# Optimization experiments

Hardware: AMD Instinct MI355X
Metric: run time of the kernel (lower is better)

## Reference

```python
import jax, jax.numpy as jnp
import numpy as np

D = 256      # model_dim
H = 8        # num_heads
S = 256      # tokens per channel
CH = [4, 2, 6, 4]  # multiplex_channels_per_sample


def _make_padding(ch, s):
    # Build gather indices / mask mapping packed tokens [T] -> padded [B, Lmax]
    B = len(ch)
    lens = [c * s for c in ch]
    T = sum(lens)
    Lmax = max(lens)
    pad_idx = np.zeros((B, Lmax), dtype=np.int32)
    pad_mask = np.zeros((B, Lmax), dtype=bool)
    off = 0
    for b, L in enumerate(lens):
        pad_idx[b, :L] = np.arange(off, off + L, dtype=np.int32)
        pad_mask[b, :L] = True
        off += L
    return jnp.asarray(pad_idx), jnp.asarray(pad_mask)


def setup_inputs() -> dict:
    key = jax.random.key(0)
    ks = jax.random.split(key, 16)
    C = sum(CH)
    x_query = jax.random.normal(ks[0], (C, S, D), jnp.float32)
    x_keyval = jax.random.normal(ks[1], (C, S, D), jnp.float32)
    pos = jax.random.normal(ks[2], (C, S, D), jnp.float32)
    pad_idx, pad_mask = _make_padding(CH, S)
    sc = 1.0 / np.sqrt(D)
    Wq = jax.random.normal(ks[3], (D, D), jnp.float32) * sc
    Wk = jax.random.normal(ks[4], (D, D), jnp.float32) * sc
    Wv = jax.random.normal(ks[5], (D, D), jnp.float32) * sc
    Wo = jax.random.normal(ks[6], (D, D), jnp.float32) * sc
    bq = jax.random.normal(ks[7], (D,), jnp.float32) * 0.02
    bk = jax.random.normal(ks[8], (D,), jnp.float32) * 0.02
    bv = jax.random.normal(ks[9], (D,), jnp.float32) * 0.02
    bo = jax.random.normal(ks[10], (D,), jnp.float32) * 0.02
    return {"x_query": x_query, "x_keyval": x_keyval, "pos": pos,
            "pad_idx": pad_idx, "pad_mask": pad_mask,
            "Wq": Wq, "bq": bq, "Wk": Wk, "bk": bk,
            "Wv": Wv, "bv": bv, "Wo": Wo, "bo": bo}


def reference(x_query, x_keyval, pos, pad_idx, pad_mask,
              Wq, bq, Wk, bk, Wv, bv, Wo, bo):
    C, s, d = x_query.shape
    T = C * s
    dh = d // H
    # MHA with positional embedding: pos is added to query and key inputs
    # (query_pos = key_pos = pos in the original forward), value is raw.
    q_in = (x_query + pos).reshape(T, d)
    k_in = (x_keyval + pos).reshape(T, d)
    v_in = x_keyval.reshape(T, d)
    q = q_in @ Wq + bq
    k = k_in @ Wk + bk
    v = v_in @ Wv + bv
    # Pad packed ragged tokens into [B, Lmax, D] per cu_seq_len segments
    B, Lmax = pad_idx.shape
    qp = q[pad_idx].reshape(B, Lmax, H, dh)
    kp = k[pad_idx].reshape(B, Lmax, H, dh)
    vp = v[pad_idx].reshape(B, Lmax, H, dh)
    scores = jnp.einsum('bqhd,bkhd->bhqk', qp, kp) / jnp.sqrt(jnp.asarray(dh, q.dtype))
    neg = jnp.asarray(jnp.finfo(scores.dtype).min, scores.dtype)
    scores = jnp.where(pad_mask[:, None, None, :], scores, neg)
    attn = jax.nn.softmax(scores, axis=-1)
    out = jnp.einsum('bhqk,bkhd->bqhd', attn, vp).reshape(B, Lmax, d)
    out = out * pad_mask[..., None]
    # Scatter padded outputs back to packed layout [T, D]
    flat = jnp.zeros((T, d), out.dtype).at[pad_idx.reshape(-1)].add(out.reshape(-1, d))
    flat = flat @ Wo + bo
    return flat.reshape(C, s, d)
```

## Files before the change

### kernel.cpp

```cpp
#include <hip/hip_runtime.h>
#include <math.h>

#define Dm 256
#define Tt 4096

typedef short  s16x8 __attribute__((ext_vector_type(8)));
typedef float  f32x4 __attribute__((ext_vector_type(4)));

__device__ __forceinline__ ushort f2bf(float x) {
    union { float f; unsigned u; } v; v.f = x;
    unsigned r = v.u + 0x7fffu + ((v.u >> 16) & 1u);
    return (ushort)(r >> 16);
}

__device__ __forceinline__ int ppos(int row, int key) {
    return row * 64 + (key & 7) + ((((key >> 3) ^ (row >> 1)) & 7) << 3);
}

__global__ __launch_bounds__(256)
void convert_x(const float* __restrict__ xq, const float* __restrict__ xkv,
               const float* __restrict__ pos,
               ushort* __restrict__ A0, ushort* __restrict__ A1, ushort* __restrict__ A2)
{
    const int t = threadIdx.x;
    const int m = blockIdx.y;
    const float* xin = (m == 0) ? xq : xkv;
    ushort* out = (m == 0) ? A0 : (m == 1) ? A1 : A2;
    const int token = blockIdx.x * 32 + (t >> 3);
    const int c0 = (t & 7) * 32;
    const float* p = &xin[token * Dm + c0];
    const float* pp = &pos[token * Dm + c0];
    #pragma unroll
    for (int i = 0; i < 4; ++i) {
        float4 fa = *(const float4*)&p[i * 8];
        float4 fb = *(const float4*)&p[i * 8 + 4];
        if (m < 2) {
            float4 pa = *(const float4*)&pp[i * 8], pb = *(const float4*)&pp[i * 8 + 4];
            fa.x += pa.x; fa.y += pa.y; fa.z += pa.z; fa.w += pa.w;
            fb.x += pb.x; fb.y += pb.y; fb.z += pb.z; fb.w += pb.w;
        }
        s16x8 v8;
        v8[0] = (short)f2bf(fa.x); v8[1] = (short)f2bf(fa.y);
        v8[2] = (short)f2bf(fa.z); v8[3] = (short)f2bf(fa.w);
        v8[4] = (short)f2bf(fb.x); v8[5] = (short)f2bf(fb.y);
        v8[6] = (short)f2bf(fb.z); v8[7] = (short)f2bf(fb.w);
        *(s16x8*)&out[token * Dm + c0 + i * 8] = v8;
    }
}

__global__ __launch_bounds__(256)
void prep_w(const float* __restrict__ Wq, const float* __restrict__ Wk,
            const float* __restrict__ Wv, const float* __restrict__ Wo,
            ushort* __restrict__ Wt)
{
    __shared__ float T[64][65];
    const int tid = threadIdx.x;
    const int m = blockIdx.y;
    const int i = blockIdx.x >> 2, j = blockIdx.x & 3;
    const float* W = (m == 0) ? Wq : (m == 1) ? Wk : (m == 2) ? Wv : Wo;

    #pragma unroll
    for (int s = 0; s < 4; ++s) {
        int idx = s * 256 + tid;
        int r = idx >> 4, c4 = (idx & 15) << 2;
        float4 f = *(const float4*)&W[(i * 64 + r) * Dm + j * 64 + c4];
        T[c4 + 0][r] = f.x; T[c4 + 1][r] = f.y;
        T[c4 + 2][r] = f.z; T[c4 + 3][r] = f.w;
    }
    __syncthreads();
    #pragma unroll
    for (int s = 0; s < 2; ++s) {
        int idx = s * 256 + tid;
        int cr = idx >> 3, k8 = (idx & 7) << 3;
        s16x8 v8;
        #pragma unroll
        for (int jj = 0; jj < 8; ++jj) v8[jj] = (short)f2bf(T[cr][k8 + jj]);
        *(s16x8*)&Wt[m * 65536 + (j * 64 + cr) * Dm + i * 64 + k8] = v8;
    }
}

__global__ __launch_bounds__(256)
void proj_gemm(const ushort* __restrict__ A0, const ushort* __restrict__ A1,
               const ushort* __restrict__ A2, const ushort* __restrict__ Wt,
               const float* __restrict__ bq, const float* __restrict__ bk,
               const float* __restrict__ bv,
               ushort* __restrict__ qo, ushort* __restrict__ ko, ushort* __restrict__ vT)
{
    __shared__ __align__(16) ushort A_s[64 * 64];
    __shared__ __align__(16) ushort B_s[64 * 64];
    const int tid = threadIdx.x;
    const int lane = tid & 63, g = lane >> 4, myrow = lane & 15, w = tid >> 6;
    const int t0 = blockIdx.x * 64;
    const int c0 = blockIdx.y * 64;
    const int m  = blockIdx.z;
    const ushort* Ab = (m == 0) ? A0 : (m == 1) ? A1 : A2;
    const ushort* WT = Wt + m * 65536;
    const float* bias = (m == 0) ? bq : (m == 1) ? bk : bv;

    f32x4 acc[4] = {};
    for (int ks = 0; ks < 4; ++ks) {
        const int k0 = ks * 64;
        #pragma unroll
        for (int s = 0; s < 2; ++s) {
            int idx = s * 256 + tid;
            int r = idx >> 3, c = idx & 7;
            *(s16x8*)&A_s[r * 64 + ((c ^ (r & 7)) << 3)] =
                *(const s16x8*)&Ab[(t0 + r) * Dm + k0 + c * 8];
            *(s16x8*)&B_s[r * 64 + ((c ^ (r & 7)) << 3)] =
                *(const s16x8*)&WT[(c0 + r) * Dm + k0 + c * 8];
        }
        __syncthreads();
        const int arow = w * 16 + myrow;
        #pragma unroll
        for (int kk = 0; kk < 2; ++kk) {
            s16x8 a = *(s16x8*)&A_s[arow * 64 + (((g + 4 * kk) ^ (arow & 7)) << 3)];
            #pragma unroll
            for (int ct = 0; ct < 4; ++ct) {
                int brow = ct * 16 + myrow;
                s16x8 b = *(s16x8*)&B_s[brow * 64 + (((g + 4 * kk) ^ (brow & 7)) << 3)];
                acc[ct] = __builtin_amdgcn_mfma_f32_16x16x32_bf16(a, b, acc[ct], 0, 0, 0);
            }
        }
        __syncthreads();
    }
    const float qsc = 0.17677669529663687f;
    #pragma unroll
    for (int ct = 0; ct < 4; ++ct) {
        int col = c0 + ct * 16 + myrow;
        float bval = bias[col];
        #pragma unroll
        for (int r = 0; r < 4; ++r) {
            int tok = t0 + w * 16 + 4 * g + r;
            float vv = acc[ct][r] + bval;
            if (m == 0)      qo[tok * Dm + col] = f2bf(vv * qsc);
            else if (m == 1) ko[tok * Dm + col] = f2bf(vv);
            else             vT[col * Tt + tok] = f2bf(vv);
        }
    }
}

__global__ __launch_bounds__(256)
void attn2(const ushort* __restrict__ q, const ushort* __restrict__ kb,
           const ushort* __restrict__ vT, ushort* __restrict__ o)
{
    __shared__ __align__(16) ushort K_s[4][64 * 32];
    __shared__ __align__(16) ushort V_s[4][32 * 64];
    __shared__ __align__(16) ushort P_s[4][16 * 64];
    const int tid = threadIdx.x;
    const int lane = tid & 63, g = lane >> 4, myrow = lane & 15, w = tid >> 6;
    const int h = blockIdx.x & 7, qt = blockIdx.x >> 3;

    int off, L;
    if (qt < 32)      { off = 0;    L = 1024; }
    else if (qt < 48) { off = 1024; L = 512;  }
    else if (qt < 96) { off = 1536; L = 1536; }
    else              { off = 3072; L = 1024; }
    const int qrow0 = qt * 32;
    const int Lw = L >> 2;
    const int kbeg = off + w * Lw;
    const int nt = Lw >> 6;

    s16x8 qf[2];
    qf[0] = *(const s16x8*)&q[(qrow0 + myrow) * Dm + h * 32 + g * 8];
    qf[1] = *(const s16x8*)&q[(qrow0 + 16 + myrow) * Dm + h * 32 + g * 8];

    f32x4 aO[2][2] = {};
    float mr[2][4], lr[2][4];
    #pragma unroll
    for (int s = 0; s < 2; ++s)
        #pragma unroll
        for (int r = 0; r < 4; ++r) { mr[s][r] = -INFINITY; lr[s][r] = 0.f; }

    s16x8 kr[4], vr[4];
    #define LOAD_TILE(kc) do {                                                          \
        int kcc = (kc);                                                                 \
        _Pragma("unroll")                                                               \
        for (int i = 0; i < 4; ++i) {                                                   \
            int idx = i * 64 + lane;                                                    \
            kr[i] = *(const s16x8*)&kb[(kcc + (idx >> 2)) * Dm + h * 32 + ((idx & 3) << 3)]; \
            vr[i] = *(const s16x8*)&vT[(h * 32 + (lane >> 3) + i * 8) * Tt + kcc + ((lane & 7) << 3)]; \
        }                                                                               \
    } while (0)

    LOAD_TILE(kbeg);
    for (int t = 0; t < nt; ++t) {
        asm volatile("s_waitcnt vmcnt(0) lgkmcnt(0)" ::: "memory");
        __builtin_amdgcn_sched_barrier(0);
        #pragma unroll
        for (int i = 0; i < 4; ++i) {
            int idx = i * 64 + lane;
            *(s16x8*)&K_s[w][(idx >> 2) * 32 + ((idx & 3) << 3)] = kr[i];
            int dh = (lane >> 3) + i * 8;
            *(s16x8*)&V_s[w][dh * 64 + (((lane & 7) ^ (dh & 7)) << 3)] = vr[i];
        }
        if (t + 1 < nt) LOAD_TILE(kbeg + (t + 1) * 64);
        asm volatile("s_waitcnt lgkmcnt(0)" ::: "memory");
        __builtin_amdgcn_sched_barrier(0);

        #pragma unroll
        for (int s = 0; s < 2; ++s) {
            const f32x4 zero = {};
            f32x4 s4[4];
            #pragma unroll
            for (int kt = 0; kt < 4; ++kt) {
                s16x8 bkf = *(const s16x8*)&K_s[w][(kt * 16 + myrow) * 32 + g * 8];
                s4[kt] = __builtin_amdgcn_mfma_f32_16x16x32_bf16(qf[s], bkf, zero, 0, 0, 0);
            }
            float mt[4], sc[4], ps[4];
            #pragma unroll
            for (int r = 0; r < 4; ++r) {
                float a = fmaxf(fmaxf(s4[0][r], s4[1][r]), fmaxf(s4[2][r], s4[3][r]));
                a = fmaxf(a, __shfl_xor(a, 1));
                a = fmaxf(a, __shfl_xor(a, 2));
                a = fmaxf(a, __shfl_xor(a, 4));
                a = fmaxf(a, __shfl_xor(a, 8));
                mt[r] = a;
            }
            #pragma unroll
            for (int r = 0; r < 4; ++r) {
                float mn = fmaxf(mr[s][r], mt[r]);
                sc[r] = __expf(mr[s][r] - mn);
                mr[s][r] = mn;
                ps[r] = 0.f;
            }
            asm volatile("s_waitcnt lgkmcnt(0)" ::: "memory");
            __builtin_amdgcn_sched_barrier(0);
            #pragma unroll
            for (int kt = 0; kt < 4; ++kt) {
                #pragma unroll
                for (int r = 0; r < 4; ++r) {
                    float p = __expf(s4[kt][r] - mr[s][r]);
                    ps[r] += p;
                    P_s[w][ppos(4 * g + r, 16 * kt + myrow)] = f2bf(p);
                }
            }
            #pragma unroll
            for (int r = 0; r < 4; ++r) {
                float sps = ps[r];
                sps += __shfl_xor(sps, 1);
                sps += __shfl_xor(sps, 2);
                sps += __shfl_xor(sps, 4);
                sps += __shfl_xor(sps, 8);
                lr[s][r] = lr[s][r] * sc[r] + sps;
                aO[s][0][r] *= sc[r];
                aO[s][1][r] *= sc[r];
            }
            asm volatile("s_waitcnt lgkmcnt(0)" ::: "memory");
            __builtin_amdgcn_sched_barrier(0);
            #pragma unroll
            for (int kk = 0; kk < 2; ++kk) {
                s16x8 ap = *(const s16x8*)&P_s[w][ppos(myrow, (g + 4 * kk) * 8)];
                s16x8 b0 = *(const s16x8*)&V_s[w][myrow * 64 + (((4 * kk + g) ^ (myrow & 7)) << 3)];
                s16x8 b1 = *(const s16x8*)&V_s[w][(16 + myrow) * 64 + (((4 * kk + g) ^ (myrow & 7)) << 3)];
                aO[s][0] = __builtin_amdgcn_mfma_f32_16x16x32_bf16(ap, b0, aO[s][0], 0, 0, 0);
                aO[s][1] = __builtin_amdgcn_mfma_f32_16x16x32_bf16(ap, b1, aO[s][1], 0, 0, 0);
            }
        }
    }
    #undef LOAD_TILE

    __syncthreads();
    float* cmb = (float*)&K_s[0][0];
    if (w > 0) {
        #pragma unroll
        for (int s = 0; s < 2; ++s)
            #pragma unroll
            for (int r = 0; r < 4; ++r) {
                int row = (w - 1) * 32 + s * 16 + 4 * g + r;
                cmb[row * 36 + myrow]      = aO[s][0][r];
                cmb[row * 36 + 16 + myrow] = aO[s][1][r];
                if (myrow == 0) { cmb[row * 36 + 32] = mr[s][r]; cmb[row * 36 + 33] = lr[s][r]; }
            }
    }
    __syncthreads();
    if (w == 0) {
        #pragma unroll
        for (int s = 0; s < 2; ++s) {
            #pragma unroll
            for (int r = 0; r < 4; ++r) {
                #pragma unroll
                for (int ww = 0; ww < 3; ++ww) {
                    int row = ww * 32 + s * 16 + 4 * g + r;
                    float m2 = cmb[row * 36 + 32], l2 = cmb[row * 36 + 33];
                    float mn = fmaxf(mr[s][r], m2);
                    float a1 = __expf(mr[s][r] - mn), a2 = __expf(m2 - mn);
                    mr[s][r] = mn;
                    lr[s][r] = lr[s][r] * a1 + l2 * a2;
                    aO[s][0][r] = aO[s][0][r] * a1 + cmb[row * 36 + myrow] * a2;
                    aO[s][1][r] = aO[s][1][r] * a1 + cmb[row * 36 + 16 + myrow] * a2;
                }
                float inv = 1.0f / lr[s][r];
                int orow = (qrow0 + s * 16 + 4 * g + r) * Dm + h * 32;
                o[orow + myrow]      = f2bf(aO[s][0][r] * inv);
                o[orow + 16 + myrow] = f2bf(aO[s][1][r] * inv);
            }
        }
    }
}

__global__ __launch_bounds__(256)
void oproj_mfma(const ushort* __restrict__ A, const ushort* __restrict__ Wt3,
                const float* __restrict__ bo, float* __restrict__ out)
{
    __shared__ __align__(16) ushort A_s[32 * 64];
    __shared__ __align__(16) ushort B_s[64 * 64];
    const int tid = threadIdx.x;
    const int lane = tid & 63, g = lane >> 4, myrow = lane & 15, w = tid >> 6;
    const int sh = w >> 1, ch = w & 1;
    const int t0 = blockIdx.x * 32;
    const int c0 = blockIdx.y * 64;

    f32x4 acc[2] = {};
    for (int ks = 0; ks < 4; ++ks) {
        const int k0 = ks * 64;
        {
            int r = tid >> 3, c = tid & 7;
            *(s16x8*)&A_s[r * 64 + ((c ^ (r & 7)) << 3)] =
                *(const s16x8*)&A[(t0 + r) * Dm + k0 + c * 8];
        }
        #pragma unroll
        for (int s = 0; s < 2; ++s) {
            int idx = s * 256 + tid;
            int r = idx >> 3, c = idx & 7;
            *(s16x8*)&B_s[r * 64 + ((c ^ (r & 7)) << 3)] =
                *(const s16x8*)&Wt3[(c0 + r) * Dm + k0 + c * 8];
        }
        __syncthreads();
        const int arow = sh * 16 + myrow;
        #pragma unroll
        for (int kk = 0; kk < 2; ++kk) {
            s16x8 a = *(s16x8*)&A_s[arow * 64 + (((g + 4 * kk) ^ (arow & 7)) << 3)];
            #pragma unroll
            for (int ct = 0; ct < 2; ++ct) {
                int brow = ch * 32 + ct * 16 + myrow;
                s16x8 b = *(s16x8*)&B_s[brow * 64 + (((g + 4 * kk) ^ (brow & 7)) << 3)];
                acc[ct] = __builtin_amdgcn_mfma_f32_16x16x32_bf16(a, b, acc[ct], 0, 0, 0);
            }
        }
        __syncthreads();
    }
    #pragma unroll
    for (int ct = 0; ct < 2; ++ct) {
        int col = c0 + ch * 32 + ct * 16 + myrow;
        float bval = bo[col];
        #pragma unroll
        for (int r = 0; r < 4; ++r)
            out[(t0 + sh * 16 + 4 * g + r) * Dm + col] = acc[ct][r] + bval;
    }
}

extern "C" void kernel_launch(void* const* d_in, const int* in_sizes, int n_in,
                              void* d_out, int out_size, void* d_ws, size_t ws_size,
                              hipStream_t stream) {
    const float* xq  = (const float*)d_in[0];
    const float* xkv = (const float*)d_in[1];
    const float* pos = (const float*)d_in[2];
    const float* Wq  = (const float*)d_in[5];
    const float* bq  = (const float*)d_in[6];
    const float* Wk  = (const float*)d_in[7];
    const float* bk  = (const float*)d_in[8];
    const float* Wv  = (const float*)d_in[9];
    const float* bv  = (const float*)d_in[10];
    const float* Wo  = (const float*)d_in[11];
    const float* bo  = (const float*)d_in[12];

    ushort* Abf = (ushort*)d_ws;
    ushort* qb  = Abf + 3 * Tt * Dm;
    ushort* kbp = qb + Tt * Dm;
    ushort* vT  = kbp + Tt * Dm;
    ushort* ab  = vT + Tt * Dm;
    ushort* Wt  = ab + Tt * Dm;

    convert_x<<<dim3(Tt / 32, 3), 256, 0, stream>>>(xq, xkv, pos, Abf,
                                                    Abf + Tt * Dm, Abf + 2 * Tt * Dm);
    prep_w<<<dim3(16, 4), 256, 0, stream>>>(Wq, Wk, Wv, Wo, Wt);
    proj_gemm<<<dim3(64, 4, 3), 256, 0, stream>>>(Abf, Abf + Tt * Dm, Abf + 2 * Tt * Dm,
                                                  Wt, bq, bk, bv, qb, kbp, vT);
    attn2<<<dim3(1024), 256, 0, stream>>>(qb, kbp, vT, ab);
    oproj_mfma<<<dim3(128, 4), 256, 0, stream>>>(ab, Wt + 3 * 65536, bo, (float*)d_out);
}
```

Measured before the change: 140.5 us.

## Load K/V MFMA fragments directly from global and add separate V transpose kernel

Attention no longer stages K and V tiles through shared memory with register prefetch. Each lane now loads its MFMA operand fragments straight from global memory. The projection GEMM writes V row-major with coalesced stores, and a new LDS-based transpose kernel produces V^T, replacing the old strided scattered stores. This trades LDS traffic and waits for direct global loads without software prefetch, and adds one extra kernel launch plus an extra V buffer round-trip.

```diff
diff --git a/kernel.cpp b/kernel.cpp
--- a/kernel.cpp
+++ b/kernel.cpp
@@ -84,7 +84,7 @@
                const ushort* __restrict__ A2, const ushort* __restrict__ Wt,
                const float* __restrict__ bq, const float* __restrict__ bk,
                const float* __restrict__ bv,
-               ushort* __restrict__ qo, ushort* __restrict__ ko, ushort* __restrict__ vT)
+               ushort* __restrict__ qo, ushort* __restrict__ ko, ushort* __restrict__ vo)
 {
     __shared__ __align__(16) ushort A_s[64 * 64];
     __shared__ __align__(16) ushort B_s[64 * 64];
@@ -96,6 +96,7 @@
     const ushort* Ab = (m == 0) ? A0 : (m == 1) ? A1 : A2;
     const ushort* WT = Wt + m * 65536;
     const float* bias = (m == 0) ? bq : (m == 1) ? bk : bv;
+    ushort* out = (m == 0) ? qo : (m == 1) ? ko : vo;
 
     f32x4 acc[4] = {};
     for (int ks = 0; ks < 4; ++ks) {
@@ -132,20 +133,46 @@
         for (int r = 0; r < 4; ++r) {
             int tok = t0 + w * 16 + 4 * g + r;
             float vv = acc[ct][r] + bval;
-            if (m == 0)      qo[tok * Dm + col] = f2bf(vv * qsc);
-            else if (m == 1) ko[tok * Dm + col] = f2bf(vv);
-            else             vT[col * Tt + tok] = f2bf(vv);
-        }
-    }
-}
-
-__global__ __launch_bounds__(256)
-void attn2(const ushort* __restrict__ q, const ushort* __restrict__ kb,
+            if (m == 0) vv *= qsc;
+            out[tok * Dm + col] = f2bf(vv);
+        }
+    }
+}
+
+__global__ __launch_bounds__(256)
+void transp_v(const ushort* __restrict__ v, ushort* __restrict__ vT)
+{
+    __shared__ __align__(16) ushort T_s[64 * 72];
+    const int tid = threadIdx.x;
+    const int t0 = blockIdx.x * 64;
+    const int c0 = blockIdx.y * 64;
+    #pragma unroll
+    for (int s = 0; s < 2; ++s) {
+        int idx = s * 256 + tid;
+        int row = idx >> 3, c8 = (idx & 7) << 3;
+        s16x8 d = *(const s16x8*)&v[(t0 + row) * Dm + c0 + c8];
+        #pragma unroll
+        for (int j = 0; j < 8; ++j) {
+            int c = c8 + j;
+            T_s[c * 72 + (row ^ ((c & 7) << 3))] = (ushort)d[j];
+        }
+    }
+    __syncthreads();
+    #pragma unroll
+    for (int s = 0; s < 2; ++s) {
+        int idx = s * 256 + tid;
+        int c = idx >> 3, k8 = (idx & 7) << 3;
+        s16x8 d = *(const s16x8*)&T_s[c * 72 + (k8 ^ ((c & 7) << 3))];
+        *(s16x8*)&vT[(c0 + c) * Tt + t0 + k8] = d;
+    }
+}
+
+__global__ __launch_bounds__(256)
+void attn3(const ushort* __restrict__ q, const ushort* __restrict__ kb,
            const ushort* __restrict__ vT, ushort* __restrict__ o)
 {
-    __shared__ __align__(16) ushort K_s[4][64 * 32];
-    __shared__ __align__(16) ushort V_s[4][32 * 64];
     __shared__ __align__(16) ushort P_s[4][16 * 64];
+    __shared__ float cmb[96 * 36];
     const int tid = threadIdx.x;
     const int lane = tid & 63, g = lane >> 4, myrow = lane & 15, w = tid >> 6;
     const int h = blockIdx.x & 7, qt = blockIdx.x >> 3;
@@ -158,7 +185,7 @@
     const int qrow0 = qt * 32;
     const int Lw = L >> 2;
     const int kbeg = off + w * Lw;
-    const int nt = Lw >> 6;
+    const int ntk = Lw >> 6;
 
     s16x8 qf[2];
     qf[0] = *(const s16x8*)&q[(qrow0 + myrow) * Dm + h * 32 + g * 8];
@@ -171,41 +198,27 @@
         #pragma unroll
         for (int r = 0; r < 4; ++r) { mr[s][r] = -INFINITY; lr[s][r] = 0.f; }
 
-    s16x8 kr[4], vr[4];
-    #define LOAD_TILE(kc) do {                                                          \
-        int kcc = (kc);                                                                 \
-        _Pragma("unroll")                                                               \
-        for (int i = 0; i < 4; ++i) {                                                   \
-            int idx = i * 64 + lane;                                                    \
-            kr[i] = *(const s16x8*)&kb[(kcc + (idx >> 2)) * Dm + h * 32 + ((idx & 3) << 3)]; \
-            vr[i] = *(const s16x8*)&vT[(h * 32 + (lane >> 3) + i * 8) * Tt + kcc + ((lane & 7) << 3)]; \
-        }                                                                               \
-    } while (0)
-
-    LOAD_TILE(kbeg);
-    for (int t = 0; t < nt; ++t) {
-        asm volatile("s_waitcnt vmcnt(0) lgkmcnt(0)" ::: "memory");
-        __builtin_amdgcn_sched_barrier(0);
-        #pragma unroll
-        for (int i = 0; i < 4; ++i) {
-            int idx = i * 64 + lane;
-            *(s16x8*)&K_s[w][(idx >> 2) * 32 + ((idx & 3) << 3)] = kr[i];
-            int dh = (lane >> 3) + i * 8;
-            *(s16x8*)&V_s[w][dh * 64 + (((lane & 7) ^ (dh & 7)) << 3)] = vr[i];
-        }
-        if (t + 1 < nt) LOAD_TILE(kbeg + (t + 1) * 64);
-        asm volatile("s_waitcnt lgkmcnt(0)" ::: "memory");
-        __builtin_amdgcn_sched_barrier(0);
+    for (int t = 0; t < ntk; ++t) {
+        const int kt0 = kbeg + t * 64;
+        s16x8 kf[4];
+        #pragma unroll
+        for (int kt = 0; kt < 4; ++kt)
+            kf[kt] = *(const s16x8*)&kb[(kt0 + kt * 16 + myrow) * Dm + h * 32 + g * 8];
+        s16x8 vfa[2], vfb[2];
+        #pragma unroll
+        for (int kk = 0; kk < 2; ++kk) {
+            vfa[kk] = *(const s16x8*)&vT[(h * 32 + myrow) * Tt + kt0 + kk * 32 + g * 8];
+            vfb[kk] = *(const s16x8*)&vT[(h * 32 + 16 + myrow) * Tt + kt0 + kk * 32 + g * 8];
+        }
 
         #pragma unroll
         for (int s = 0; s < 2; ++s) {
             const f32x4 zero = {};
             f32x4 s4[4];
             #pragma unroll
-            for (int kt = 0; kt < 4; ++kt) {
-                s16x8 bkf = *(const s16x8*)&K_s[w][(kt * 16 + myrow) * 32 + g * 8];
-                s4[kt] = __builtin_amdgcn_mfma_f32_16x16x32_bf16(qf[s], bkf, zero, 0, 0, 0);
-            }
+            for (int kt = 0; kt < 4; ++kt)
+                s4[kt] = __builtin_amdgcn_mfma_f32_16x16x32_bf16(qf[s], kf[kt], zero, 0, 0, 0);
+
             float mt[4], sc[4], ps[4];
             #pragma unroll
             for (int r = 0; r < 4; ++r) {
@@ -250,17 +263,13 @@
             #pragma unroll
             for (int kk = 0; kk < 2; ++kk) {
                 s16x8 ap = *(const s16x8*)&P_s[w][ppos(myrow, (g + 4 * kk) * 8)];
-                s16x8 b0 = *(const s16x8*)&V_s[w][myrow * 64 + (((4 * kk + g) ^ (myrow & 7)) << 3)];
-                s16x8 b1 = *(const s16x8*)&V_s[w][(16 + myrow) * 64 + (((4 * kk + g) ^ (myrow & 7)) << 3)];
-                aO[s][0] = __builtin_amdgcn_mfma_f32_16x16x32_bf16(ap, b0, aO[s][0], 0, 0, 0);
-                aO[s][1] = __builtin_amdgcn_mfma_f32_16x16x32_bf16(ap, b1, aO[s][1], 0, 0, 0);
-            }
-        }
-    }
-    #undef LOAD_TILE
+                aO[s][0] = __builtin_amdgcn_mfma_f32_16x16x32_bf16(ap, vfa[kk], aO[s][0], 0, 0, 0);
+                aO[s][1] = __builtin_amdgcn_mfma_f32_16x16x32_bf16(ap, vfb[kk], aO[s][1], 0, 0, 0);
+            }
+        }
+    }
 
     __syncthreads();
-    float* cmb = (float*)&K_s[0][0];
     if (w > 0) {
         #pragma unroll
         for (int s = 0; s < 2; ++s)
@@ -367,15 +376,17 @@
     ushort* Abf = (ushort*)d_ws;
     ushort* qb  = Abf + 3 * Tt * Dm;
     ushort* kbp = qb + Tt * Dm;
-    ushort* vT  = kbp + Tt * Dm;
-    ushort* ab  = vT + Tt * Dm;
+    ushort* vb  = kbp + Tt * Dm;
+    ushort* vTt = vb + Tt * Dm;
+    ushort* ab  = vTt + Tt * Dm;
     ushort* Wt  = ab + Tt * Dm;
 
     convert_x<<<dim3(Tt / 32, 3), 256, 0, stream>>>(xq, xkv, pos, Abf,
                                                     Abf + Tt * Dm, Abf + 2 * Tt * Dm);
     prep_w<<<dim3(16, 4), 256, 0, stream>>>(Wq, Wk, Wv, Wo, Wt);
     proj_gemm<<<dim3(64, 4, 3), 256, 0, stream>>>(Abf, Abf + Tt * Dm, Abf + 2 * Tt * Dm,
-                                                  Wt, bq, bk, bv, qb, kbp, vT);
-    attn2<<<dim3(1024), 256, 0, stream>>>(qb, kbp, vT, ab);
+                                                  Wt, bq, bk, bv, qb, kbp, vb);
+    transp_v<<<dim3(64, 4), 256, 0, stream>>>(vb, vTt);
+    attn3<<<dim3(1024), 256, 0, stream>>>(qb, kbp, vTt, ab);
     oproj_mfma<<<dim3(128, 4), 256, 0, stream>>>(ab, Wt + 3 * 65536, bo, (float*)d_out);
 }
```

New measurement: 135.1 us. 3.8% less time.
